# Optimization experiments

Hardware: AMD Instinct MI355X
Metric: run time of the kernel (lower is better)

## Reference

```python
import jax, jax.numpy as jnp
import numpy as np

B, S, D = 4, 2048, 1024
H = 16
DH = D // H  # attention_head_size = 64


def setup_inputs() -> dict:
    key = jax.random.key(0)
    ks = jax.random.split(key, 7)
    scale = 0.02
    return {
        "hidden_states": jax.random.normal(ks[0], (B, S, D), dtype=jnp.float32),
        "Wq": jax.random.normal(ks[1], (D, D), dtype=jnp.float32) * scale,
        "bq": jnp.zeros((D,), dtype=jnp.float32),
        "Wk": jax.random.normal(ks[2], (D, D), dtype=jnp.float32) * scale,
        "bk": jnp.zeros((D,), dtype=jnp.float32),
        "Wv": jax.random.normal(ks[3], (D, D), dtype=jnp.float32) * scale,
        "bv": jnp.zeros((D,), dtype=jnp.float32),
    }


def _split_heads(x):
    # [B, S, D] -> [B, H, S, DH]
    b, s, _ = x.shape
    return x.reshape(b, s, H, DH).transpose(0, 2, 1, 3)


def reference(hidden_states, Wq, bq, Wk, bk, Wv, bv):
    # torch nn.Linear computes x @ W.T + b
    q = _split_heads(hidden_states @ Wq.T + bq)  # [B,H,S,DH]
    k = _split_heads(hidden_states @ Wk.T + bk)
    v = _split_heads(hidden_states @ Wv.T + bv)

    scores = jnp.einsum("bhqd,bhkd->bhqk", q, k) / jnp.sqrt(jnp.float32(DH))
    # original detaches attention probs (LRP-style)
    probs = jax.lax.stop_gradient(jax.nn.softmax(scores, axis=-1))
    ctx = jnp.einsum("bhqk,bhkd->bhqd", probs, v)  # [B,H,S,DH]
    # [B,H,S,DH] -> [B,S,D]
    return ctx.transpose(0, 2, 1, 3).reshape(hidden_states.shape[0], hidden_states.shape[1], D)
```

## Files before the change

kernel.cpp:

```cpp
#include <hip/hip_runtime.h>

typedef _Float16 f16;
typedef f16 f16x2 __attribute__((ext_vector_type(2)));
typedef f16 f16x4 __attribute__((ext_vector_type(4)));
typedef f16 f16x8 __attribute__((ext_vector_type(8)));
typedef float f32x4 __attribute__((ext_vector_type(4)));

#define NB 4
#define NS 2048
#define ND 1024
#define NH 16
#define NDH 64

__device__ __forceinline__ void gl2lds16(const void* g, void* l) {
  __builtin_amdgcn_global_load_lds(
      (const __attribute__((address_space(1))) unsigned int*)g,
      (__attribute__((address_space(3))) unsigned int*)l, 16, 0, 0);
}

__device__ __forceinline__ float fast_exp2(float x) {
  return __builtin_amdgcn_exp2f(x);
}

__device__ __forceinline__ f16x2 pk_f16(float a, float b) {
  return __builtin_bit_cast(f16x2, __builtin_amdgcn_cvt_pkrtz(a, b));
}

__global__ __launch_bounds__(256) void cvt_all(
    const float* __restrict__ X, const float* __restrict__ Wq,
    const float* __restrict__ Wk, const float* __restrict__ Wv,
    f16* __restrict__ Xh, f16* __restrict__ Wh) {
  int b = blockIdx.x;
  const float* src;
  f16* dst;
  int off;
  if (b < 8192)       { src = X;  dst = Xh;               off = 0; }
  else if (b < 9216)  { src = Wq; dst = Wh;               off = 8192; }
  else if (b < 10240) { src = Wk; dst = Wh + (1u << 20);  off = 9216; }
  else                { src = Wv; dst = Wh + (2u << 20);  off = 10240; }
  int i = (b - off) * 256 + threadIdx.x;
  float4 v = ((const float4*)src)[i];
  f16x4 h = {(f16)v.x, (f16)v.y, (f16)v.z, (f16)v.w};
  ((f16x4*)dst)[i] = h;
}

__global__ __launch_bounds__(256) void qkv_gemm(
    const f16* __restrict__ Xh, const f16* __restrict__ Wh,
    const float* __restrict__ bq, const float* __restrict__ bk,
    const float* __restrict__ bv,
    f16* __restrict__ QF, f16* __restrict__ KF, f16* __restrict__ VF) {
  __shared__ f16 Ah[2][128 * 64];
  __shared__ f16 Bh[2][128 * 64];
  const int t = threadIdx.x;
  const int tileM = blockIdx.x * 128;
  const int nGlob = blockIdx.y * 128;
  const int mat = nGlob >> 10;
  const int col0 = nGlob & 1023;
  const int wave = t >> 6, lane = t & 63;
  const int mOff = (wave & 1) * 64, nOff = (wave >> 1) * 64;
  const int lr = lane & 15, quad = lane >> 4;

  f32x4 acc[4][4];
#pragma unroll
  for (int i = 0; i < 4; i++)
#pragma unroll
    for (int j = 0; j < 4; j++) acc[i][j] = f32x4{0.f, 0.f, 0.f, 0.f};

  const int srow = t >> 3;
  const int sx = ((t & 7) ^ (srow & 7)) * 8;
  const f16* ag = Xh + (size_t)(tileM + srow) * ND + sx;
  const f16* bg = Wh + (size_t)mat * ND * ND + (size_t)(col0 + srow) * ND + sx;
  const bool qk = (mat < 2);
  const int rx = lr & 7;

  gl2lds16(ag,                       Ah[0] + t * 8);
  gl2lds16(ag + (size_t)32 * ND,     Ah[0] + 2048 + t * 8);
  gl2lds16(ag + (size_t)64 * ND,     Ah[0] + 4096 + t * 8);
  gl2lds16(ag + (size_t)96 * ND,     Ah[0] + 6144 + t * 8);
  gl2lds16(bg,                       Bh[0] + t * 8);
  gl2lds16(bg + (size_t)32 * ND,     Bh[0] + 2048 + t * 8);
  gl2lds16(bg + (size_t)64 * ND,     Bh[0] + 4096 + t * 8);
  gl2lds16(bg + (size_t)96 * ND,     Bh[0] + 6144 + t * 8);
  asm volatile("s_waitcnt vmcnt(0)" ::: "memory");
  __builtin_amdgcn_s_barrier();

  for (int kk = 0; kk < 16; ++kk) {
    const int buf = kk & 1;
    if (kk < 15) {
      const size_t ko = (size_t)(kk + 1) * 64;
      gl2lds16(ag + ko,                       Ah[buf ^ 1] + t * 8);
      gl2lds16(ag + (size_t)32 * ND + ko,     Ah[buf ^ 1] + 2048 + t * 8);
      gl2lds16(ag + (size_t)64 * ND + ko,     Ah[buf ^ 1] + 4096 + t * 8);
      gl2lds16(ag + (size_t)96 * ND + ko,     Ah[buf ^ 1] + 6144 + t * 8);
      gl2lds16(bg + ko,                       Bh[buf ^ 1] + t * 8);
      gl2lds16(bg + (size_t)32 * ND + ko,     Bh[buf ^ 1] + 2048 + t * 8);
      gl2lds16(bg + (size_t)64 * ND + ko,     Bh[buf ^ 1] + 4096 + t * 8);
      gl2lds16(bg + (size_t)96 * ND + ko,     Bh[buf ^ 1] + 6144 + t * 8);
    }
#pragma unroll
    for (int c = 0; c < 2; c++) {
      const int ch = ((c * 4 + quad) ^ rx) * 8;
      f16x8 af[4], bf[4];
#pragma unroll
      for (int i = 0; i < 4; i++)
        af[i] = *(const f16x8*)(Ah[buf] + (mOff + i * 16 + lr) * 64 + ch);
#pragma unroll
      for (int j = 0; j < 4; j++)
        bf[j] = *(const f16x8*)(Bh[buf] + (nOff + j * 16 + lr) * 64 + ch);
      if (qk) {
#pragma unroll
        for (int i = 0; i < 4; i++)
#pragma unroll
          for (int j = 0; j < 4; j++)
            acc[i][j] = __builtin_amdgcn_mfma_f32_16x16x32_f16(bf[j], af[i], acc[i][j], 0, 0, 0);
      } else {
#pragma unroll
        for (int i = 0; i < 4; i++)
#pragma unroll
          for (int j = 0; j < 4; j++)
            acc[i][j] = __builtin_amdgcn_mfma_f32_16x16x32_f16(af[i], bf[j], acc[i][j], 0, 0, 0);
      }
    }
    asm volatile("s_waitcnt vmcnt(0)" ::: "memory");
    __builtin_amdgcn_s_barrier();
  }

  if (qk) {
    const float* bias = (mat == 0) ? bq : bk;
    f16* dst = (mat == 0) ? QF : KF;
    const float sc = (mat == 0) ? 0.18033688f : 1.0f;
    const int jstart = (quad & 1) * 4;
#pragma unroll
    for (int j = 0; j < 4; j++) {
      int n0 = col0 + nOff + j * 16;
      int h = n0 >> 6;
      int f = j >> 1;
      int lam = lr + 16 * ((2 * j + (quad >> 1)) & 3);
      float4 bb = *(const float4*)(bias + n0 + quad * 4);
#pragma unroll
      for (int i = 0; i < 4; i++) {
        int sF = tileM + mOff + i * 16;
        int b = sF >> 11, st = (sF & 2047) >> 4;
        int bh = b * NH + h;
        f16x4 v;
#pragma unroll
        for (int r = 0; r < 4; r++) v[r] = (f16)((acc[i][j][r] + (&bb.x)[r]) * sc);
        *(f16x4*)(dst + (((size_t)(bh * 128 + st) * 2 + f) * 64 + lam) * 8 + jstart) = v;
      }
    }
  } else {
#pragma unroll
    for (int j = 0; j < 4; j++) {
      int n = col0 + nOff + j * 16 + lr;
      int h = n >> 6, dt = (n >> 4) & 3;
      float bb = bv[n];
#pragma unroll
      for (int p = 0; p < 2; p++) {
        int i0 = 2 * p;
        int sF = tileM + mOff + i0 * 16;
        int b = sF >> 11;
        int kt2 = (sF & 2047) >> 5;
        int bh = b * NH + h;
        f16x8 v;
#pragma unroll
        for (int r = 0; r < 4; r++) {
          v[r] = (f16)(acc[i0][j][r] + bb);
          v[4 + r] = (f16)(acc[i0 + 1][j][r] + bb);
        }
        *(f16x8*)(VF + ((size_t)(bh * 64 + kt2) * 4 + dt) * 512 +
                  (size_t)(quad * 16 + lr) * 8) = v;
      }
    }
  }
}

__global__ __launch_bounds__(256, 2) void attn_kernel(
    const f16* __restrict__ QF, const f16* __restrict__ KF,
    const f16* __restrict__ VF, float* __restrict__ out) {
  __shared__ f16 LK[3][2048];
  __shared__ f16 LV[3][2048];
  const int t = threadIdx.x, wave = t >> 6, lane = t & 63;
  const int lr = lane & 15, quad = lane >> 4;
  const int bh = blockIdx.x, qb = blockIdx.y;
  const int bb = bh >> 4, hh = bh & 15;
  const size_t bhOff = (size_t)bh * 131072;
  const f16* Qp = QF + bhOff + (size_t)lane * 8;
  const f16* Kg = KF + bhOff + (size_t)t * 8;
  const f16* Vg = VF + bhOff + (size_t)t * 8;
  const int st0 = qb * 16 + wave * 4;

  f16x8 qf[4][2];
#pragma unroll
  for (int qt = 0; qt < 4; qt++) {
    qf[qt][0] = *(const f16x8*)(Qp + (size_t)(st0 + qt) * 1024);
    qf[qt][1] = *(const f16x8*)(Qp + (size_t)(st0 + qt) * 1024 + 512);
  }

  f32x4 o[4][4];
#pragma unroll
  for (int qt = 0; qt < 4; qt++)
#pragma unroll
    for (int dt = 0; dt < 4; dt++) o[qt][dt] = f32x4{0.f, 0.f, 0.f, 0.f};
  f32x4 lacc[4];
#pragma unroll
  for (int qt = 0; qt < 4; qt++) lacc[qt] = f32x4{0.f, 0.f, 0.f, 0.f};
  const f16x8 ones8 = {(f16)1.f, (f16)1.f, (f16)1.f, (f16)1.f,
                       (f16)1.f, (f16)1.f, (f16)1.f, (f16)1.f};

  f16x8 pfP[4], vvP[4];

  gl2lds16(Kg,        &LK[0][t * 8]);
  gl2lds16(Vg,        &LV[0][t * 8]);
  gl2lds16(Kg + 2048, &LK[1][t * 8]);
  gl2lds16(Vg + 2048, &LV[1][t * 8]);
  asm volatile("s_waitcnt vmcnt(2)" ::: "memory");
  __builtin_amdgcn_s_barrier();

  {
    f16x8 kk[4];
#pragma unroll
    for (int i = 0; i < 4; i++)
      kk[i] = *(const f16x8*)(&LK[0][i * 512 + lane * 8]);
#pragma unroll
    for (int i = 0; i < 4; i++)
      vvP[i] = *(const f16x8*)(&LV[0][i * 512 + lane * 8]);
    gl2lds16(Kg + 2 * 2048, &LK[2][t * 8]);
    gl2lds16(Vg + 2 * 2048, &LV[2][t * 8]);
    f32x4 sA[4], sB[4];
#pragma unroll
    for (int qt = 0; qt < 4; qt++) {
      sA[qt] = f32x4{0.f, 0.f, 0.f, 0.f};
      sA[qt] = __builtin_amdgcn_mfma_f32_16x16x32_f16(kk[0], qf[qt][0], sA[qt], 0, 0, 0);
      sA[qt] = __builtin_amdgcn_mfma_f32_16x16x32_f16(kk[1], qf[qt][1], sA[qt], 0, 0, 0);
      sB[qt] = f32x4{0.f, 0.f, 0.f, 0.f};
      sB[qt] = __builtin_amdgcn_mfma_f32_16x16x32_f16(kk[2], qf[qt][0], sB[qt], 0, 0, 0);
      sB[qt] = __builtin_amdgcn_mfma_f32_16x16x32_f16(kk[3], qf[qt][1], sB[qt], 0, 0, 0);
    }
#pragma unroll
    for (int qt = 0; qt < 4; qt++) {
      f16x2 a0 = pk_f16(fast_exp2(sA[qt][0]), fast_exp2(sA[qt][1]));
      f16x2 a1 = pk_f16(fast_exp2(sA[qt][2]), fast_exp2(sA[qt][3]));
      f16x2 b0 = pk_f16(fast_exp2(sB[qt][0]), fast_exp2(sB[qt][1]));
      f16x2 b1 = pk_f16(fast_exp2(sB[qt][2]), fast_exp2(sB[qt][3]));
      f16x4 lo = __builtin_shufflevector(a0, a1, 0, 1, 2, 3);
      f16x4 hi = __builtin_shufflevector(b0, b1, 0, 1, 2, 3);
      pfP[qt] = __builtin_shufflevector(lo, hi, 0, 1, 2, 3, 4, 5, 6, 7);
    }
  }
  asm volatile("s_waitcnt vmcnt(2)" ::: "memory");
  __builtin_amdgcn_s_barrier();

  int cur = 1;
  for (int g = 1; g < 64; ++g) {
    f16x8 kk[4], vv[4];
#pragma unroll
    for (int i = 0; i < 4; i++)
      kk[i] = *(const f16x8*)(&LK[cur][i * 512 + lane * 8]);
#pragma unroll
    for (int i = 0; i < 4; i++)
      vv[i] = *(const f16x8*)(&LV[cur][i * 512 + lane * 8]);
    {
      int s2 = cur + 2; if (s2 >= 3) s2 -= 3;
      const size_t nk = (size_t)((g + 2) & 63) * 2048;
      gl2lds16(Kg + nk, &LK[s2][t * 8]);
      gl2lds16(Vg + nk, &LV[s2][t * 8]);
    }
    __builtin_amdgcn_s_setprio(1);
#pragma unroll
    for (int dt = 0; dt < 4; dt++)
#pragma unroll
      for (int qt = 0; qt < 4; qt++)
        o[qt][dt] = __builtin_amdgcn_mfma_f32_16x16x32_f16(pfP[qt], vvP[dt], o[qt][dt], 0, 0, 0);
#pragma unroll
    for (int qt = 0; qt < 4; qt++)
      lacc[qt] = __builtin_amdgcn_mfma_f32_16x16x32_f16(pfP[qt], ones8, lacc[qt], 0, 0, 0);
    f32x4 sA[4], sB[4];
#pragma unroll
    for (int qt = 0; qt < 4; qt++) {
      sA[qt] = f32x4{0.f, 0.f, 0.f, 0.f};
      sA[qt] = __builtin_amdgcn_mfma_f32_16x16x32_f16(kk[0], qf[qt][0], sA[qt], 0, 0, 0);
      sA[qt] = __builtin_amdgcn_mfma_f32_16x16x32_f16(kk[1], qf[qt][1], sA[qt], 0, 0, 0);
      sB[qt] = f32x4{0.f, 0.f, 0.f, 0.f};
      sB[qt] = __builtin_amdgcn_mfma_f32_16x16x32_f16(kk[2], qf[qt][0], sB[qt], 0, 0, 0);
      sB[qt] = __builtin_amdgcn_mfma_f32_16x16x32_f16(kk[3], qf[qt][1], sB[qt], 0, 0, 0);
    }
    __builtin_amdgcn_s_setprio(0);
#pragma unroll
    for (int qt = 0; qt < 4; qt++) {
      f16x2 a0 = pk_f16(fast_exp2(sA[qt][0]), fast_exp2(sA[qt][1]));
      f16x2 a1 = pk_f16(fast_exp2(sA[qt][2]), fast_exp2(sA[qt][3]));
      f16x2 b0 = pk_f16(fast_exp2(sB[qt][0]), fast_exp2(sB[qt][1]));
      f16x2 b1 = pk_f16(fast_exp2(sB[qt][2]), fast_exp2(sB[qt][3]));
      f16x4 lo = __builtin_shufflevector(a0, a1, 0, 1, 2, 3);
      f16x4 hi = __builtin_shufflevector(b0, b1, 0, 1, 2, 3);
      pfP[qt] = __builtin_shufflevector(lo, hi, 0, 1, 2, 3, 4, 5, 6, 7);
    }
#pragma unroll
    for (int i = 0; i < 4; i++) vvP[i] = vv[i];
    asm volatile("s_waitcnt vmcnt(2)" ::: "memory");
    __builtin_amdgcn_s_barrier();
    cur = (cur == 2) ? 0 : cur + 1;
  }

#pragma unroll
  for (int dt = 0; dt < 4; dt++)
#pragma unroll
    for (int qt = 0; qt < 4; qt++)
      o[qt][dt] = __builtin_amdgcn_mfma_f32_16x16x32_f16(pfP[qt], vvP[dt], o[qt][dt], 0, 0, 0);
#pragma unroll
  for (int qt = 0; qt < 4; qt++)
    lacc[qt] = __builtin_amdgcn_mfma_f32_16x16x32_f16(pfP[qt], ones8, lacc[qt], 0, 0, 0);

#pragma unroll
  for (int qt = 0; qt < 4; qt++) {
#pragma unroll
    for (int r = 0; r < 4; r++) {
      float inv = 1.0f / lacc[qt][r];
      int q = qb * 256 + wave * 64 + qt * 16 + quad * 4 + r;
#pragma unroll
      for (int dt = 0; dt < 4; dt++)
        out[((size_t)bb * NS + q) * ND + hh * 64 + dt * 16 + lr] = o[qt][dt][r] * inv;
    }
  }
}

extern "C" void kernel_launch(void* const* d_in, const int* in_sizes, int n_in,
                              void* d_out, int out_size, void* d_ws, size_t ws_size,
                              hipStream_t stream) {
  const float* X  = (const float*)d_in[0];
  const float* Wq = (const float*)d_in[1];
  const float* bq = (const float*)d_in[2];
  const float* Wk = (const float*)d_in[3];
  const float* bk = (const float*)d_in[4];
  const float* Wv = (const float*)d_in[5];
  const float* bv = (const float*)d_in[6];
  float* out = (float*)d_out;

  f16* Xh = (f16*)d_ws;
  f16* Wh = (f16*)((char*)d_ws + (size_t)(16u << 20));
  f16* QF = (f16*)((char*)d_ws + (size_t)(22u << 20));
  f16* KF = (f16*)((char*)d_ws + (size_t)(38u << 20));
  f16* VF = (f16*)((char*)d_ws + (size_t)(54u << 20));

  cvt_all<<<11264, 256, 0, stream>>>(X, Wq, Wk, Wv, Xh, Wh);
  qkv_gemm<<<dim3(64, 24), 256, 0, stream>>>(Xh, Wh, bq, bk, bv, QF, KF, VF);
  attn_kernel<<<dim3(64, 8), 256, 0, stream>>>(QF, KF, VF, out);
}
```

Before: 215.2 us.

## Process two KV tiles per barrier with a six-stage LDS ring

The attention main loop now handles two 32-key tiles per iteration and synchronises once per pair instead of once per tile. The LDS ring for K/V grows from three to six stages with a prefetch distance of four tiles. Inside each iteration the second tile's QK^T and exp are interleaved with the first tile's PV MFMAs to overlap more work. This halves the barrier count but doubles LDS use and raises register pressure, which may reduce occupancy at two blocks per CU.

```diff
diff --git a/kernel.cpp b/kernel.cpp
--- a/kernel.cpp
+++ b/kernel.cpp
@@ -177,8 +177,8 @@
 __global__ __launch_bounds__(256, 2) void attn_kernel(
     const f16* __restrict__ QF, const f16* __restrict__ KF,
     const f16* __restrict__ VF, float* __restrict__ out) {
-  __shared__ f16 LK[3][2048];
-  __shared__ f16 LV[3][2048];
+  __shared__ f16 LK[6][2048];
+  __shared__ f16 LV[6][2048];
   const int t = threadIdx.x, wave = t >> 6, lane = t & 63;
   const int lr = lane & 15, quad = lane >> 4;
   const int bh = blockIdx.x, qb = blockIdx.y;
@@ -209,61 +209,96 @@
 
   f16x8 pfP[4], vvP[4];
 
-  gl2lds16(Kg,        &LK[0][t * 8]);
-  gl2lds16(Vg,        &LV[0][t * 8]);
-  gl2lds16(Kg + 2048, &LK[1][t * 8]);
-  gl2lds16(Vg + 2048, &LV[1][t * 8]);
-  asm volatile("s_waitcnt vmcnt(2)" ::: "memory");
+#pragma unroll
+  for (int g = 0; g < 4; ++g) {
+    gl2lds16(Kg + (size_t)g * 2048, &LK[g][t * 8]);
+    gl2lds16(Vg + (size_t)g * 2048, &LV[g][t * 8]);
+  }
+  asm volatile("s_waitcnt vmcnt(4)" ::: "memory");
   __builtin_amdgcn_s_barrier();
 
   {
-    f16x8 kk[4];
-#pragma unroll
-    for (int i = 0; i < 4; i++)
-      kk[i] = *(const f16x8*)(&LK[0][i * 512 + lane * 8]);
-#pragma unroll
-    for (int i = 0; i < 4; i++)
-      vvP[i] = *(const f16x8*)(&LV[0][i * 512 + lane * 8]);
-    gl2lds16(Kg + 2 * 2048, &LK[2][t * 8]);
-    gl2lds16(Vg + 2 * 2048, &LV[2][t * 8]);
-    f32x4 sA[4], sB[4];
-#pragma unroll
-    for (int qt = 0; qt < 4; qt++) {
-      sA[qt] = f32x4{0.f, 0.f, 0.f, 0.f};
-      sA[qt] = __builtin_amdgcn_mfma_f32_16x16x32_f16(kk[0], qf[qt][0], sA[qt], 0, 0, 0);
-      sA[qt] = __builtin_amdgcn_mfma_f32_16x16x32_f16(kk[1], qf[qt][1], sA[qt], 0, 0, 0);
-      sB[qt] = f32x4{0.f, 0.f, 0.f, 0.f};
-      sB[qt] = __builtin_amdgcn_mfma_f32_16x16x32_f16(kk[2], qf[qt][0], sB[qt], 0, 0, 0);
-      sB[qt] = __builtin_amdgcn_mfma_f32_16x16x32_f16(kk[3], qf[qt][1], sB[qt], 0, 0, 0);
-    }
-#pragma unroll
-    for (int qt = 0; qt < 4; qt++) {
-      f16x2 a0 = pk_f16(fast_exp2(sA[qt][0]), fast_exp2(sA[qt][1]));
-      f16x2 a1 = pk_f16(fast_exp2(sA[qt][2]), fast_exp2(sA[qt][3]));
-      f16x2 b0 = pk_f16(fast_exp2(sB[qt][0]), fast_exp2(sB[qt][1]));
-      f16x2 b1 = pk_f16(fast_exp2(sB[qt][2]), fast_exp2(sB[qt][3]));
+    f16x8 kkA[4], vvA[4];
+#pragma unroll
+    for (int k2 = 0; k2 < 4; k2++) kkA[k2] = *(const f16x8*)(&LK[0][k2 * 512 + lane * 8]);
+#pragma unroll
+    for (int k2 = 0; k2 < 4; k2++) vvA[k2] = *(const f16x8*)(&LV[0][k2 * 512 + lane * 8]);
+    gl2lds16(Kg + (size_t)4 * 2048, &LK[4][t * 8]);
+    gl2lds16(Vg + (size_t)4 * 2048, &LV[4][t * 8]);
+    gl2lds16(Kg + (size_t)5 * 2048, &LK[5][t * 8]);
+    gl2lds16(Vg + (size_t)5 * 2048, &LV[5][t * 8]);
+    f32x4 s0[4], s1[4];
+#pragma unroll
+    for (int qt = 0; qt < 4; qt++) {
+      s0[qt] = f32x4{0.f, 0.f, 0.f, 0.f};
+      s0[qt] = __builtin_amdgcn_mfma_f32_16x16x32_f16(kkA[0], qf[qt][0], s0[qt], 0, 0, 0);
+      s0[qt] = __builtin_amdgcn_mfma_f32_16x16x32_f16(kkA[1], qf[qt][1], s0[qt], 0, 0, 0);
+      s1[qt] = f32x4{0.f, 0.f, 0.f, 0.f};
+      s1[qt] = __builtin_amdgcn_mfma_f32_16x16x32_f16(kkA[2], qf[qt][0], s1[qt], 0, 0, 0);
+      s1[qt] = __builtin_amdgcn_mfma_f32_16x16x32_f16(kkA[3], qf[qt][1], s1[qt], 0, 0, 0);
+    }
+    f16x8 kkB[4], vvB[4];
+#pragma unroll
+    for (int k2 = 0; k2 < 4; k2++) kkB[k2] = *(const f16x8*)(&LK[1][k2 * 512 + lane * 8]);
+#pragma unroll
+    for (int k2 = 0; k2 < 4; k2++) vvB[k2] = *(const f16x8*)(&LV[1][k2 * 512 + lane * 8]);
+    f16x8 pfA;
+#pragma unroll
+    for (int qt = 0; qt < 4; qt++) {
+      f16x2 a0 = pk_f16(fast_exp2(s0[qt][0]), fast_exp2(s0[qt][1]));
+      f16x2 a1 = pk_f16(fast_exp2(s0[qt][2]), fast_exp2(s0[qt][3]));
+      f16x2 b0 = pk_f16(fast_exp2(s1[qt][0]), fast_exp2(s1[qt][1]));
+      f16x2 b1 = pk_f16(fast_exp2(s1[qt][2]), fast_exp2(s1[qt][3]));
+      f16x4 lo = __builtin_shufflevector(a0, a1, 0, 1, 2, 3);
+      f16x4 hi = __builtin_shufflevector(b0, b1, 0, 1, 2, 3);
+      pfA = __builtin_shufflevector(lo, hi, 0, 1, 2, 3, 4, 5, 6, 7);
+#pragma unroll
+      for (int dt = 0; dt < 4; dt++)
+        o[qt][dt] = __builtin_amdgcn_mfma_f32_16x16x32_f16(pfA, vvA[dt], o[qt][dt], 0, 0, 0);
+      lacc[qt] = __builtin_amdgcn_mfma_f32_16x16x32_f16(pfA, ones8, lacc[qt], 0, 0, 0);
+    }
+    f32x4 t0[4], t1[4];
+#pragma unroll
+    for (int qt = 0; qt < 4; qt++) {
+      t0[qt] = f32x4{0.f, 0.f, 0.f, 0.f};
+      t0[qt] = __builtin_amdgcn_mfma_f32_16x16x32_f16(kkB[0], qf[qt][0], t0[qt], 0, 0, 0);
+      t0[qt] = __builtin_amdgcn_mfma_f32_16x16x32_f16(kkB[1], qf[qt][1], t0[qt], 0, 0, 0);
+      t1[qt] = f32x4{0.f, 0.f, 0.f, 0.f};
+      t1[qt] = __builtin_amdgcn_mfma_f32_16x16x32_f16(kkB[2], qf[qt][0], t1[qt], 0, 0, 0);
+      t1[qt] = __builtin_amdgcn_mfma_f32_16x16x32_f16(kkB[3], qf[qt][1], t1[qt], 0, 0, 0);
+    }
+#pragma unroll
+    for (int qt = 0; qt < 4; qt++) {
+      f16x2 a0 = pk_f16(fast_exp2(t0[qt][0]), fast_exp2(t0[qt][1]));
+      f16x2 a1 = pk_f16(fast_exp2(t0[qt][2]), fast_exp2(t0[qt][3]));
+      f16x2 b0 = pk_f16(fast_exp2(t1[qt][0]), fast_exp2(t1[qt][1]));
+      f16x2 b1 = pk_f16(fast_exp2(t1[qt][2]), fast_exp2(t1[qt][3]));
       f16x4 lo = __builtin_shufflevector(a0, a1, 0, 1, 2, 3);
       f16x4 hi = __builtin_shufflevector(b0, b1, 0, 1, 2, 3);
       pfP[qt] = __builtin_shufflevector(lo, hi, 0, 1, 2, 3, 4, 5, 6, 7);
     }
-  }
-  asm volatile("s_waitcnt vmcnt(2)" ::: "memory");
-  __builtin_amdgcn_s_barrier();
-
-  int cur = 1;
-  for (int g = 1; g < 64; ++g) {
-    f16x8 kk[4], vv[4];
-#pragma unroll
-    for (int i = 0; i < 4; i++)
-      kk[i] = *(const f16x8*)(&LK[cur][i * 512 + lane * 8]);
-#pragma unroll
-    for (int i = 0; i < 4; i++)
-      vv[i] = *(const f16x8*)(&LV[cur][i * 512 + lane * 8]);
+#pragma unroll
+    for (int k2 = 0; k2 < 4; k2++) vvP[k2] = vvB[k2];
+    asm volatile("s_waitcnt vmcnt(4)" ::: "memory");
+    __builtin_amdgcn_s_barrier();
+  }
+
+  for (int i = 1; i < 32; ++i) {
+    const int ga = 2 * i, gb = 2 * i + 1;
+    const int bA = ga % 6, bB = gb % 6;
+    f16x8 kkA[4], vvA[4];
+#pragma unroll
+    for (int k2 = 0; k2 < 4; k2++) kkA[k2] = *(const f16x8*)(&LK[bA][k2 * 512 + lane * 8]);
+#pragma unroll
+    for (int k2 = 0; k2 < 4; k2++) vvA[k2] = *(const f16x8*)(&LV[bA][k2 * 512 + lane * 8]);
     {
-      int s2 = cur + 2; if (s2 >= 3) s2 -= 3;
-      const size_t nk = (size_t)((g + 2) & 63) * 2048;
-      gl2lds16(Kg + nk, &LK[s2][t * 8]);
-      gl2lds16(Vg + nk, &LV[s2][t * 8]);
+      const int sa = (ga + 4) % 6, sb = (gb + 4) % 6;
+      const size_t oa = (size_t)((ga + 4) & 63) * 2048;
+      const size_t ob = (size_t)((gb + 4) & 63) * 2048;
+      gl2lds16(Kg + oa, &LK[sa][t * 8]);
+      gl2lds16(Vg + oa, &LV[sa][t * 8]);
+      gl2lds16(Kg + ob, &LK[sb][t * 8]);
+      gl2lds16(Vg + ob, &LV[sb][t * 8]);
     }
     __builtin_amdgcn_s_setprio(1);
 #pragma unroll
@@ -274,32 +309,60 @@
 #pragma unroll
     for (int qt = 0; qt < 4; qt++)
       lacc[qt] = __builtin_amdgcn_mfma_f32_16x16x32_f16(pfP[qt], ones8, lacc[qt], 0, 0, 0);
-    f32x4 sA[4], sB[4];
-#pragma unroll
-    for (int qt = 0; qt < 4; qt++) {
-      sA[qt] = f32x4{0.f, 0.f, 0.f, 0.f};
-      sA[qt] = __builtin_amdgcn_mfma_f32_16x16x32_f16(kk[0], qf[qt][0], sA[qt], 0, 0, 0);
-      sA[qt] = __builtin_amdgcn_mfma_f32_16x16x32_f16(kk[1], qf[qt][1], sA[qt], 0, 0, 0);
-      sB[qt] = f32x4{0.f, 0.f, 0.f, 0.f};
-      sB[qt] = __builtin_amdgcn_mfma_f32_16x16x32_f16(kk[2], qf[qt][0], sB[qt], 0, 0, 0);
-      sB[qt] = __builtin_amdgcn_mfma_f32_16x16x32_f16(kk[3], qf[qt][1], sB[qt], 0, 0, 0);
+    f32x4 s0[4], s1[4];
+#pragma unroll
+    for (int qt = 0; qt < 4; qt++) {
+      s0[qt] = f32x4{0.f, 0.f, 0.f, 0.f};
+      s0[qt] = __builtin_amdgcn_mfma_f32_16x16x32_f16(kkA[0], qf[qt][0], s0[qt], 0, 0, 0);
+      s0[qt] = __builtin_amdgcn_mfma_f32_16x16x32_f16(kkA[1], qf[qt][1], s0[qt], 0, 0, 0);
+      s1[qt] = f32x4{0.f, 0.f, 0.f, 0.f};
+      s1[qt] = __builtin_amdgcn_mfma_f32_16x16x32_f16(kkA[2], qf[qt][0], s1[qt], 0, 0, 0);
+      s1[qt] = __builtin_amdgcn_mfma_f32_16x16x32_f16(kkA[3], qf[qt][1], s1[qt], 0, 0, 0);
     }
     __builtin_amdgcn_s_setprio(0);
-#pragma unroll
-    for (int qt = 0; qt < 4; qt++) {
-      f16x2 a0 = pk_f16(fast_exp2(sA[qt][0]), fast_exp2(sA[qt][1]));
-      f16x2 a1 = pk_f16(fast_exp2(sA[qt][2]), fast_exp2(sA[qt][3]));
-      f16x2 b0 = pk_f16(fast_exp2(sB[qt][0]), fast_exp2(sB[qt][1]));
-      f16x2 b1 = pk_f16(fast_exp2(sB[qt][2]), fast_exp2(sB[qt][3]));
+    f16x8 kkB[4], vvB[4];
+#pragma unroll
+    for (int k2 = 0; k2 < 4; k2++) kkB[k2] = *(const f16x8*)(&LK[bB][k2 * 512 + lane * 8]);
+#pragma unroll
+    for (int k2 = 0; k2 < 4; k2++) vvB[k2] = *(const f16x8*)(&LV[bB][k2 * 512 + lane * 8]);
+#pragma unroll
+    for (int qt = 0; qt < 4; qt++) {
+      f16x2 a0 = pk_f16(fast_exp2(s0[qt][0]), fast_exp2(s0[qt][1]));
+      f16x2 a1 = pk_f16(fast_exp2(s0[qt][2]), fast_exp2(s0[qt][3]));
+      f16x2 b0 = pk_f16(fast_exp2(s1[qt][0]), fast_exp2(s1[qt][1]));
+      f16x2 b1 = pk_f16(fast_exp2(s1[qt][2]), fast_exp2(s1[qt][3]));
+      f16x4 lo = __builtin_shufflevector(a0, a1, 0, 1, 2, 3);
+      f16x4 hi = __builtin_shufflevector(b0, b1, 0, 1, 2, 3);
+      f16x8 pfA = __builtin_shufflevector(lo, hi, 0, 1, 2, 3, 4, 5, 6, 7);
+#pragma unroll
+      for (int dt = 0; dt < 4; dt++)
+        o[qt][dt] = __builtin_amdgcn_mfma_f32_16x16x32_f16(pfA, vvA[dt], o[qt][dt], 0, 0, 0);
+      lacc[qt] = __builtin_amdgcn_mfma_f32_16x16x32_f16(pfA, ones8, lacc[qt], 0, 0, 0);
+    }
+    f32x4 t0[4], t1[4];
+#pragma unroll
+    for (int qt = 0; qt < 4; qt++) {
+      t0[qt] = f32x4{0.f, 0.f, 0.f, 0.f};
+      t0[qt] = __builtin_amdgcn_mfma_f32_16x16x32_f16(kkB[0], qf[qt][0], t0[qt], 0, 0, 0);
+      t0[qt] = __builtin_amdgcn_mfma_f32_16x16x32_f16(kkB[1], qf[qt][1], t0[qt], 0, 0, 0);
+      t1[qt] = f32x4{0.f, 0.f, 0.f, 0.f};
+      t1[qt] = __builtin_amdgcn_mfma_f32_16x16x32_f16(kkB[2], qf[qt][0], t1[qt], 0, 0, 0);
+      t1[qt] = __builtin_amdgcn_mfma_f32_16x16x32_f16(kkB[3], qf[qt][1], t1[qt], 0, 0, 0);
+    }
+#pragma unroll
+    for (int qt = 0; qt < 4; qt++) {
+      f16x2 a0 = pk_f16(fast_exp2(t0[qt][0]), fast_exp2(t0[qt][1]));
+      f16x2 a1 = pk_f16(fast_exp2(t0[qt][2]), fast_exp2(t0[qt][3]));
+      f16x2 b0 = pk_f16(fast_exp2(t1[qt][0]), fast_exp2(t1[qt][1]));
+      f16x2 b1 = pk_f16(fast_exp2(t1[qt][2]), fast_exp2(t1[qt][3]));
       f16x4 lo = __builtin_shufflevector(a0, a1, 0, 1, 2, 3);
       f16x4 hi = __builtin_shufflevector(b0, b1, 0, 1, 2, 3);
       pfP[qt] = __builtin_shufflevector(lo, hi, 0, 1, 2, 3, 4, 5, 6, 7);
     }
 #pragma unroll
-    for (int i = 0; i < 4; i++) vvP[i] = vv[i];
-    asm volatile("s_waitcnt vmcnt(2)" ::: "memory");
+    for (int k2 = 0; k2 < 4; k2++) vvP[k2] = vvB[k2];
+    asm volatile("s_waitcnt vmcnt(4)" ::: "memory");
     __builtin_amdgcn_s_barrier();
-    cur = (cur == 2) ? 0 : cur + 1;
   }
 
 #pragma unroll
```

Result: no change. 215.6 us (+0.2%).
